# Kernel optimization log

Hardware: AMD Instinct MI355X
Metric: run time of the kernel (lower is better)

Reference implementation:

```python
import jax, jax.numpy as jnp
import numpy as np

L = 4          # num transformer layers
C = 128        # embed_dim
P = 16         # patch size
NH = 8         # num heads
HD = C // NH   # head dim
SCALE = HD ** -0.5
THRESH = [0.001, 0.0012, 0.0015, 0.002]
EPS = 1e-5


def _ln(x, w, b):
    mu = jnp.mean(x, -1, keepdims=True)
    v = jnp.mean(jnp.square(x - mu), -1, keepdims=True)
    return (x - mu) * jax.lax.rsqrt(v + EPS) * w + b


def _attn(x, qw, qb, ow, ob):
    B, N, _ = x.shape
    qkv = (x @ qw + qb).reshape(B, N, 3, NH, HD)
    q, k, v = jnp.moveaxis(qkv, 2, 0)                      # each [B,N,NH,HD]
    q = q.transpose(0, 2, 1, 3)
    k = k.transpose(0, 2, 1, 3)
    v = v.transpose(0, 2, 1, 3)                            # [B,NH,N,HD]
    probs = jax.nn.softmax(jnp.einsum('bhnd,bhmd->bhnm', q, k) * SCALE, axis=-1)
    o = jnp.einsum('bhnm,bhmd->bhnd', probs, v).transpose(0, 2, 1, 3).reshape(B, N, C)
    return o @ ow + ob, probs


def _layer(x, i, ln1_w, ln1_b, qkv_w, qkv_b, out_w, out_b, ln2_w, ln2_b, w1, b1, w2, b2):
    a, probs = _attn(_ln(x, ln1_w[i], ln1_b[i]), qkv_w[i], qkv_b[i], out_w[i], out_b[i])
    x = x + a
    h = jax.nn.gelu(_ln(x, ln2_w[i], ln2_b[i]) @ w1[i] + b1[i], approximate=False)
    return x + h @ w2[i] + b2[i], probs


def forward(conv_w, conv_b, cls_token, pos_embed, ln1_w, ln1_b, qkv_w, qkv_b,
            out_w, out_b, ln2_w, ln2_b, mlp_w1, mlp_b1, mlp_w2, mlp_b2, x, meta=None):
    B = x.shape[0]
    Hh, Ww = x.shape[2] // P, x.shape[3] // P
    # patch embed == conv with kernel=stride=P, expressed as a patch matmul
    xr = x.reshape(B, 3, Hh, P, Ww, P).transpose(0, 2, 4, 1, 3, 5).reshape(B, Hh * Ww, 3 * P * P)
    tok = xr @ conv_w.reshape(C, -1).T + conv_b           # [B, nH*nW, C]
    x = jnp.concatenate([jnp.broadcast_to(cls_token, (B, 1, C)), tok], axis=1) + pos_embed
    meta_out = []
    for i in range(L):
        x, probs = _layer(x, i, ln1_w, ln1_b, qkv_w, qkv_b, out_w, out_b,
                          ln2_w, ln2_b, mlp_w1, mlp_b1, mlp_w2, mlp_b2)
        if i < L - 1:
            cls_t, tokens = x[:, :1], x[:, 1:]
            if meta is None:
                am = jnp.mean(probs[:, :, 1:, 0], axis=1)  # [B, N] attn of tokens to cls
                keep = am > THRESH[i]
                fb = keep.sum(1) == 0                      # fallback: keep argmax token
                keep = keep | (fb[:, None] & (jnp.arange(am.shape[1])[None, :] == jnp.argmax(am, 1)[:, None]))
                count = keep.sum(1)
                order = jnp.argsort(~keep, axis=1)         # stable: kept tokens first, in order
                mk = int(jnp.max(count))
                order, count = np.asarray(order), np.asarray(count)
                meta_out.append((order, count, mk))
            else:
                order, count, mk = meta[i]
            g = jnp.take_along_axis(tokens, jnp.asarray(order[:, :mk])[:, :, None], axis=1)
            valid = (jnp.arange(mk)[None, :] < jnp.asarray(count)[:, None]).astype(tokens.dtype)
            x = jnp.concatenate([cls_t, g * valid[:, :, None]], axis=1)
            # original re-adds pos_embed[0:1+mk] regardless of which tokens survived
            x = x + jnp.concatenate([pos_embed[:, :1], pos_embed[:, 1:1 + mk]], axis=1)
    return x, meta_out


def setup_inputs() -> dict:
    key = jax.random.key(0)
    ks = jax.random.split(key, 8)
    def w(k, shape, fan_in):
        return jax.random.normal(k, shape, jnp.float32) / np.float32(np.sqrt(fan_in))
    N_POS = (512 // P) * (512 // P) + 1  # 1025
    return {
        'conv_w': w(ks[0], (C, 3, P, P), 3 * P * P),
        'conv_b': jnp.zeros((C,), jnp.float32),
        'cls_token': jnp.zeros((1, 1, C), jnp.float32),
        'pos_embed': 0.02 * jax.random.truncated_normal(ks[1], -2.0, 2.0, (1, N_POS, C), jnp.float32),
        'ln1_w': jnp.ones((L, C), jnp.float32), 'ln1_b': jnp.zeros((L, C), jnp.float32),
        'qkv_w': w(ks[2], (L, C, 3 * C), C), 'qkv_b': jnp.zeros((L, 3 * C), jnp.float32),
        'out_w': w(ks[3], (L, C, C), C), 'out_b': jnp.zeros((L, C), jnp.float32),
        'ln2_w': jnp.ones((L, C), jnp.float32), 'ln2_b': jnp.zeros((L, C), jnp.float32),
        'mlp_w1': w(ks[4], (L, C, 4 * C), C), 'mlp_b1': jnp.zeros((L, 4 * C), jnp.float32),
        'mlp_w2': w(ks[5], (L, 4 * C, C), 4 * C), 'mlp_b2': jnp.zeros((L, C), jnp.float32),
        'x': jax.random.normal(ks[6], (8, 3, 512, 512), jnp.float32),
    }


def reference(conv_w, conv_b, cls_token, pos_embed, ln1_w, ln1_b, qkv_w, qkv_b,
              out_w, out_b, ln2_w, ln2_b, mlp_w1, mlp_b1, mlp_w2, mlp_b2, x):
    out, _ = forward(conv_w, conv_b, cls_token, pos_embed, ln1_w, ln1_b, qkv_w, qkv_b,
                     out_w, out_b, ln2_w, ln2_b, mlp_w1, mlp_b1, mlp_w2, mlp_b2, x)
    return out
```

## Files before the change

kernel.cpp:

```cpp
#include <hip/hip_runtime.h>
#include <hip/hip_bf16.h>
#include <math.h>

typedef __hip_bfloat16 bf16;
typedef __attribute__((ext_vector_type(4))) _Float16 half4;
typedef __attribute__((ext_vector_type(4))) float f32x4;

#define NMAX 1025
#define TMAX 1024
#define BATCH 8
#define CH 128
#define NHEAD 8
#define HDIM 16
#define MMAX (BATCH * NMAX)
#define QTILES 65
#define VSTRIDE 1028
#define POSZ 1049600
#define KCHUNK 192

__device__ __forceinline__ float b2f(bf16 v) { return __bfloat162float(v); }

__device__ __forceinline__ bool is_bf16(const void* ln1w_raw) {
    return ((const unsigned*)ln1w_raw)[0] == 0x3F803F80u;
}
__device__ __forceinline__ float ldsel(const void* p, size_t i, bool bf) {
    return bf ? __bfloat162float(((const bf16*)p)[i]) : ((const float*)p)[i];
}

struct CvtDesc { const void* src; float* dst; int cnt; };
struct CvtPack { CvtDesc d[15]; };

__global__ void convert_kernel(CvtPack p, const void* ln1w_raw, int* nTok) {
    bool bf = is_bf16(ln1w_raw);
    CvtDesc dd = p.d[blockIdx.y];
    int idx = blockIdx.x * 256 + threadIdx.x;
    if (idx < dd.cnt) dd.dst[idx] = ldsel(dd.src, idx, bf);
    if (blockIdx.y == 0 && idx == 0) nTok[0] = NMAX;
}

__global__ void prep_kernel(const void* conv_w, float* __restrict__ wT,
                            const void* ln1w_raw) {
    bool bf = is_bf16(ln1w_raw);
    int idx = blockIdx.x * 256 + threadIdx.x;
    if (idx < 768 * 128) {
        int k = idx >> 7, oc = idx & 127;
        wT[idx] = ldsel(conv_w, (size_t)oc * 768 + k, bf);
    }
}

__global__ __launch_bounds__(256) void patch_partial(
        const void* __restrict__ img, const float* __restrict__ wT,
        float* __restrict__ partial, const void* ln1w_raw) {
    __shared__ float pbuf[8 * KCHUNK];
    bool bf = is_bf16(ln1w_raw);
    int b = blockIdx.y;
    int g = blockIdx.x & 127;
    int kc = blockIdx.x >> 7;
    int tid = threadIdx.x;
    int t0 = g * 8;
    int kbase = kc * KCHUNK;
    const int NV = 8 * KCHUNK / 4;
    for (int i = tid; i < NV; i += 256) {
        int e = i << 2;
        int t = e / KCHUNK, kloc = e - t * KCHUNK;
        int k = kbase + kloc;
        int c = k >> 8, rem = k & 255, p1 = rem >> 4, p2 = rem & 15;
        int hw = t0 + t;
        int h = hw >> 5, w = hw & 31;
        size_t a = (((size_t)(b * 3 + c) * 512) + h * 16 + p1) * 512 + w * 16 + p2;
        float4 v;
        if (bf) {
            ushort4 u = *(const ushort4*)((const unsigned short*)img + a);
            v.x = __uint_as_float((unsigned)u.x << 16);
            v.y = __uint_as_float((unsigned)u.y << 16);
            v.z = __uint_as_float((unsigned)u.z << 16);
            v.w = __uint_as_float((unsigned)u.w << 16);
        } else {
            v = *(const float4*)((const float*)img + a);
        }
        *(float4*)&pbuf[e] = v;
    }
    __syncthreads();
    int team = tid >> 7;
    int col = tid & 127;
    float acc[4];
#pragma unroll
    for (int t = 0; t < 4; t++) acc[t] = 0.f;
    const float* wc = wT + (size_t)kbase * 128;
    const float* pb = pbuf + team * 4 * KCHUNK;
    for (int k4 = 0; k4 < KCHUNK; k4 += 4) {
        float w0 = wc[(k4 + 0) * 128 + col];
        float w1 = wc[(k4 + 1) * 128 + col];
        float w2 = wc[(k4 + 2) * 128 + col];
        float w3 = wc[(k4 + 3) * 128 + col];
#pragma unroll
        for (int t = 0; t < 4; t++) {
            const float4 a = *(const float4*)&pb[t * KCHUNK + k4];
            acc[t] = fmaf(a.x, w0, acc[t]);
            acc[t] = fmaf(a.y, w1, acc[t]);
            acc[t] = fmaf(a.z, w2, acc[t]);
            acc[t] = fmaf(a.w, w3, acc[t]);
        }
    }
    float* pp = partial + ((size_t)(kc * 8 + b) * 1024 + t0 + team * 4) * 128 + col;
#pragma unroll
    for (int t = 0; t < 4; t++) pp[(size_t)t * 128] = acc[t];
}

__global__ __launch_bounds__(256) void patch_reduce(
        const float* __restrict__ partial, const float* __restrict__ conv_b,
        const float* __restrict__ cls_tok, const float* __restrict__ pos,
        float* __restrict__ out) {
    if (blockIdx.x == 4096) {
        for (int i = threadIdx.x; i < 8 * 128; i += 256) {
            int b = i >> 7, c = i & 127;
            out[(size_t)(b * NMAX) * CH + c] = cls_tok[c] + pos[c];
        }
        return;
    }
    int idx = blockIdx.x * 256 + threadIdx.x;
    int tg = idx >> 7;
    int col = idx & 127;
    int b = tg >> 10, tok = tg & 1023;
    size_t pi = ((size_t)b * 1024 + tok) * 128 + col;
    const size_t PSTRIDE = (size_t)8 * 1024 * 128;
    float v = partial[pi] + partial[pi + PSTRIDE]
            + partial[pi + 2 * PSTRIDE] + partial[pi + 3 * PSTRIDE];
    out[((size_t)(b * NMAX) + 1 + tok) * CH + col] =
        v + conv_b[col] + pos[(size_t)(1 + tok) * CH + col];
}

template <int K, int NCOL, int CTILE, int ROWS, int TEAMS, bool LN,
          bool GELU_ACT, bool RESID, bool QKV_SPLIT>
__global__ void mm_kernel(const float* __restrict__ A, const float* __restrict__ W,
                          const float* __restrict__ bias, const float* __restrict__ lnw,
                          const float* __restrict__ lnb, const float* __restrict__ R,
                          float* __restrict__ out, _Float16* __restrict__ kout,
                          _Float16* __restrict__ vout, const int* __restrict__ nPtr) {
    __shared__ float As[ROWS * K];
    const int THREADS = CTILE * TEAMS;
    const int RPT = ROWS / TEAMS;
    int N = nPtr[0];
    int M = BATCH * N;
    int row0 = blockIdx.x * ROWS;
    if (row0 >= M) return;
    int tid = threadIdx.x;
    for (int i = tid; i < ROWS * K / 4; i += THREADS) {
        int e = i << 2;
        int r = e / K, rem = e % K;
        float4 v;
        int row = row0 + r;
        if (row < M)
            v = *(const float4*)&A[(size_t)row * K + rem];
        else
            v = make_float4(0.f, 0.f, 0.f, 0.f);
        *(float4*)&As[r * K + rem] = v;
    }
    __syncthreads();
    if (LN) {
        int wid = tid >> 6, lane = tid & 63;
        const int NW = THREADS / 64;
        float wl0 = lnw[lane], wl1 = lnw[64 + lane];
        float bl0 = lnb[lane], bl1 = lnb[64 + lane];
        for (int r = wid; r < ROWS; r += NW) {
            float x0 = As[r * K + lane], x1 = As[r * K + 64 + lane];
            float s = x0 + x1;
#pragma unroll
            for (int off = 32; off; off >>= 1) s += __shfl_xor(s, off);
            float mu = s * (1.f / 128.f);
            float d0 = x0 - mu, d1 = x1 - mu;
            float v = d0 * d0 + d1 * d1;
#pragma unroll
            for (int off = 32; off; off >>= 1) v += __shfl_xor(v, off);
            float inv = 1.f / sqrtf(v * (1.f / 128.f) + 1e-5f);
            As[r * K + lane] = d0 * inv * wl0 + bl0;
            As[r * K + 64 + lane] = d1 * inv * wl1 + bl1;
        }
        __syncthreads();
    }
    int team = tid / CTILE;
    int col = tid % CTILE;
    const float* At = As + team * RPT * K;
    float acc[RPT];
#pragma unroll
    for (int r = 0; r < RPT; r++) acc[r] = 0.f;
    for (int k4 = 0; k4 < K; k4 += 4) {
        float w0 = W[(size_t)(k4 + 0) * NCOL + col];
        float w1 = W[(size_t)(k4 + 1) * NCOL + col];
        float w2 = W[(size_t)(k4 + 2) * NCOL + col];
        float w3 = W[(size_t)(k4 + 3) * NCOL + col];
#pragma unroll
        for (int r = 0; r < RPT; r++) {
            const float4 a = *(const float4*)&At[r * K + k4];
            acc[r] = fmaf(a.x, w0, acc[r]);
            acc[r] = fmaf(a.y, w1, acc[r]);
            acc[r] = fmaf(a.z, w2, acc[r]);
            acc[r] = fmaf(a.w, w3, acc[r]);
        }
    }
    float bv = bias[col];
    int rbase = row0 + team * RPT;
    int rmax = min(RPT, M - rbase);
    if (QKV_SPLIT) {
        int part = col >> 7;
        int c128 = col & 127;
        int hh = c128 >> 4, dd = c128 & 15;
        for (int r = 0; r < rmax; r++) {
            float v = acc[r] + bv;
            int row = rbase + r;
            if (part == 0) {
                out[(size_t)row * 128 + c128] = v;
            } else {
                int bb = row / N, nn = row - (row / N) * N;
                if (part == 1) {
                    _Float16 hi = (_Float16)v;
                    _Float16 lo = (_Float16)(v - (float)hi);
                    size_t kb2 = ((size_t)(bb * 8 + hh) * NMAX + nn) * 32 + dd;
                    kout[kb2] = hi;
                    kout[kb2 + 16] = lo;
                } else {
                    vout[((size_t)(bb * 8 + hh) * 16 + dd) * VSTRIDE + nn] = (_Float16)v;
                }
            }
        }
        if (blockIdx.x == 0 && part == 2) {
            int zn = min(16, VSTRIDE - N);
            for (int bb = 0; bb < 8; bb++) {
                size_t rb = ((size_t)((bb * 8 + hh) * 16 + dd)) * VSTRIDE;
                for (int i = 0; i < zn; i++) vout[rb + N + i] = (_Float16)0.f;
            }
            if (hh == 7 && dd == 15) {
                for (int i = 0; i < 16; i++)
                    vout[(size_t)1024 * VSTRIDE + i] = (_Float16)0.f;
            }
        }
    } else {
        for (int r = 0; r < rmax; r++) {
            float v = acc[r] + bv;
            if (GELU_ACT) v = 0.5f * v * (1.f + erff(v * 0.70710678118654752f));
            if (RESID) v += R[(size_t)(rbase + r) * NCOL + col];
            out[(size_t)(rbase + r) * NCOL + col] = v;
        }
    }
}

__global__ __launch_bounds__(256) void attn_kernel(
        const float* __restrict__ qbuf, const _Float16* __restrict__ kbuf,
        const _Float16* __restrict__ vbuf, float* __restrict__ oout,
        float* __restrict__ clsp, const int* __restrict__ nPtr) {
    __shared__ float sO[3][64][4];
    __shared__ float sL[3][64];
    __shared__ float sM[3][16];
    int N = nPtr[0];
    int bid = blockIdx.x;
    int b = bid & 7;
    int h = (bid >> 3) & 7;
    int qt = bid >> 6;
    if (qt * 16 >= N) return;
    int wave = threadIdx.x >> 6;
    int lane = threadIdx.x & 63;
    int ql = lane & 15;
    int hig = lane >> 4;
    int nq = qt * 16 + ql;
    int nqc = min(nq, N - 1);
    half4 qhi, qlo;
    {
        const float4 qv = *(const float4*)(qbuf + ((size_t)(b * N + nqc)) * 128 + h * HDIM + hig * 4);
        float q0 = qv.x * 0.25f, q1 = qv.y * 0.25f, q2 = qv.z * 0.25f, q3 = qv.w * 0.25f;
        qhi[0] = (_Float16)q0; qlo[0] = (_Float16)(q0 - (float)qhi[0]);
        qhi[1] = (_Float16)q1; qlo[1] = (_Float16)(q1 - (float)qhi[1]);
        qhi[2] = (_Float16)q2; qlo[2] = (_Float16)(q2 - (float)qhi[2]);
        qhi[3] = (_Float16)q3; qlo[3] = (_Float16)(q3 - (float)qhi[3]);
    }
    const _Float16* kb = kbuf + (size_t)(b * 8 + h) * NMAX * 32;
    const _Float16* vt = vbuf + ((size_t)(b * 8 + h) * 16 + ql) * VSTRIDE;
    f32x4 of = {0.f, 0.f, 0.f, 0.f};
    const f32x4 zz = {0.f, 0.f, 0.f, 0.f};
    float m = -3.0e38f, l = 0.f, s0raw = 0.f;
    int ntAll = (N + 15) >> 4;
    int ntFull = N >> 4;
    int nqt = (ntAll + 3) >> 2;
    int t0h = wave * nqt;
    int t1h = min(ntAll, t0h + nqt);
    int fullEnd = min(t1h, ntFull);
    int t = t0h;
    for (; t + 2 <= fullEnd; t += 2) {
        int k0 = t * 16;
        const _Float16* kpA = kb + ((size_t)(k0 + ql)) * 32 + hig * 4;
        const _Float16* kpB = kpA + 16 * 32;
        half4 khiA = *(const half4*)(kpA);
        half4 kloA = *(const half4*)(kpA + 16);
        half4 khiB = *(const half4*)(kpB);
        half4 kloB = *(const half4*)(kpB + 16);
        f32x4 sA1 = __builtin_amdgcn_mfma_f32_16x16x16f16(khiA, qhi, zz, 0, 0, 0);
        f32x4 sB1 = __builtin_amdgcn_mfma_f32_16x16x16f16(khiB, qhi, zz, 0, 0, 0);
        f32x4 sA2 = __builtin_amdgcn_mfma_f32_16x16x16f16(khiA, qlo, zz, 0, 0, 0);
        f32x4 sB2 = __builtin_amdgcn_mfma_f32_16x16x16f16(khiB, qlo, zz, 0, 0, 0);
        sA2 = __builtin_amdgcn_mfma_f32_16x16x16f16(kloA, qhi, sA2, 0, 0, 0);
        sB2 = __builtin_amdgcn_mfma_f32_16x16x16f16(kloB, qhi, sB2, 0, 0, 0);
        f32x4 saA = sA1 + sA2;
        f32x4 saB = sB1 + sB2;
        if (t == 0) s0raw = saA[0];
        float mcA = fmaxf(fmaxf(saA[0], saA[1]), fmaxf(saA[2], saA[3]));
        float mcB = fmaxf(fmaxf(saB[0], saB[1]), fmaxf(saB[2], saB[3]));
        float mloc = fmaxf(mcA, mcB);
        if (!__all(mloc <= m + 8.f)) {
            float mc = fmaxf(mloc, __shfl_xor(mloc, 16));
            mc = fmaxf(mc, __shfl_xor(mc, 32));
            float mnew = fmaxf(m, mc);
            float corr = __expf(m - mnew);
            l *= corr;
#pragma unroll
            for (int r = 0; r < 4; r++)
                of[r] *= __shfl(corr, hig * 4 + r);
            m = mnew;
        }
        float pA0 = __expf(saA[0] - m), pA1 = __expf(saA[1] - m);
        float pA2 = __expf(saA[2] - m), pA3 = __expf(saA[3] - m);
        float pB0 = __expf(saB[0] - m), pB1 = __expf(saB[1] - m);
        float pB2 = __expf(saB[2] - m), pB3 = __expf(saB[3] - m);
        l += ((pA0 + pA1) + (pA2 + pA3)) + ((pB0 + pB1) + (pB2 + pB3));
        half4 pfA, pfB;
        pfA[0] = (_Float16)pA0; pfA[1] = (_Float16)pA1;
        pfA[2] = (_Float16)pA2; pfA[3] = (_Float16)pA3;
        pfB[0] = (_Float16)pB0; pfB[1] = (_Float16)pB1;
        pfB[2] = (_Float16)pB2; pfB[3] = (_Float16)pB3;
        half4 vfA = *(const half4*)(vt + k0 + hig * 4);
        half4 vfB = *(const half4*)(vt + k0 + 16 + hig * 4);
        of = __builtin_amdgcn_mfma_f32_16x16x16f16(pfA, vfA, of, 0, 0, 0);
        of = __builtin_amdgcn_mfma_f32_16x16x16f16(pfB, vfB, of, 0, 0, 0);
    }
    if (t < fullEnd) {
        int k0 = t * 16;
        const _Float16* kp = kb + ((size_t)(k0 + ql)) * 32 + hig * 4;
        half4 khi = *(const half4*)(kp);
        half4 klo = *(const half4*)(kp + 16);
        f32x4 s1 = __builtin_amdgcn_mfma_f32_16x16x16f16(khi, qhi, zz, 0, 0, 0);
        f32x4 s2 = __builtin_amdgcn_mfma_f32_16x16x16f16(khi, qlo, zz, 0, 0, 0);
        s2 = __builtin_amdgcn_mfma_f32_16x16x16f16(klo, qhi, s2, 0, 0, 0);
        f32x4 sa = s1 + s2;
        if (t == 0) s0raw = sa[0];
        float mloc = fmaxf(fmaxf(sa[0], sa[1]), fmaxf(sa[2], sa[3]));
        if (!__all(mloc <= m + 8.f)) {
            float mc = fmaxf(mloc, __shfl_xor(mloc, 16));
            mc = fmaxf(mc, __shfl_xor(mc, 32));
            float mnew = fmaxf(m, mc);
            float corr = __expf(m - mnew);
            l *= corr;
#pragma unroll
            for (int r = 0; r < 4; r++)
                of[r] *= __shfl(corr, hig * 4 + r);
            m = mnew;
        }
        float p0 = __expf(sa[0] - m), p1 = __expf(sa[1] - m);
        float p2 = __expf(sa[2] - m), p3 = __expf(sa[3] - m);
        l += (p0 + p1) + (p2 + p3);
        half4 pf;
        pf[0] = (_Float16)p0; pf[1] = (_Float16)p1;
        pf[2] = (_Float16)p2; pf[3] = (_Float16)p3;
        half4 vf = *(const half4*)(vt + k0 + hig * 4);
        of = __builtin_amdgcn_mfma_f32_16x16x16f16(pf, vf, of, 0, 0, 0);
        t++;
    }
    if (t < t1h) {
        int k0t = t * 16;
        int kk = min(k0t + ql, N - 1);
        const _Float16* kp = kb + (size_t)kk * 32 + hig * 4;
        half4 khi = *(const half4*)(kp);
        half4 klo = *(const half4*)(kp + 16);
        f32x4 s1 = __builtin_amdgcn_mfma_f32_16x16x16f16(khi, qhi, zz, 0, 0, 0);
        f32x4 s2 = __builtin_amdgcn_mfma_f32_16x16x16f16(khi, qlo, zz, 0, 0, 0);
        s2 = __builtin_amdgcn_mfma_f32_16x16x16f16(klo, qhi, s2, 0, 0, 0);
        f32x4 sa = s1 + s2;
        if (t == 0) s0raw = sa[0];
        float s0 = (k0t + hig * 4 + 0 < N) ? sa[0] : -3.0e38f;
        float s1m = (k0t + hig * 4 + 1 < N) ? sa[1] : -3.0e38f;
        float s2m = (k0t + hig * 4 + 2 < N) ? sa[2] : -3.0e38f;
        float s3m = (k0t + hig * 4 + 3 < N) ? sa[3] : -3.0e38f;
        float mloc = fmaxf(fmaxf(s0, s1m), fmaxf(s2m, s3m));
        if (!__all(mloc <= m + 8.f)) {
            float mc = fmaxf(mloc, __shfl_xor(mloc, 16));
            mc = fmaxf(mc, __shfl_xor(mc, 32));
            float mnew = fmaxf(m, mc);
            float corr = __expf(m - mnew);
            l *= corr;
#pragma unroll
            for (int r = 0; r < 4; r++)
                of[r] *= __shfl(corr, hig * 4 + r);
            m = mnew;
        }
        float p0 = __expf(s0 - m);
        float p1 = __expf(s1m - m);
        float p2 = __expf(s2m - m);
        float p3 = __expf(s3m - m);
        l += (p0 + p1) + (p2 + p3);
        half4 pf;
        pf[0] = (_Float16)p0; pf[1] = (_Float16)p1;
        pf[2] = (_Float16)p2; pf[3] = (_Float16)p3;
        half4 vf = *(const half4*)(vt + k0t + hig * 4);
        of = __builtin_amdgcn_mfma_f32_16x16x16f16(pf, vf, of, 0, 0, 0);
    }
    l += __shfl_xor(l, 16);
    l += __shfl_xor(l, 32);
    if (wave != 0) {
        if (hig == 0) sM[wave - 1][ql] = m;
        sL[wave - 1][lane] = l;
        sO[wave - 1][lane][0] = of[0];
        sO[wave - 1][lane][1] = of[1];
        sO[wave - 1][lane][2] = of[2];
        sO[wave - 1][lane][3] = of[3];
    }
    __syncthreads();
    if (wave == 0) {
        float m1 = sM[0][ql], m2 = sM[1][ql], m3 = sM[2][ql];
        float M = fmaxf(fmaxf(m, m1), fmaxf(m2, m3));
        float w0 = __expf(m - M), w1 = __expf(m1 - M);
        float w2 = __expf(m2 - M), w3 = __expf(m3 - M);
        float L = w0 * l + w1 * sL[0][lane] + w2 * sL[1][lane] + w3 * sL[2][lane];
        float linv = 1.f / L;
#pragma unroll
        for (int r = 0; r < 4; r++) {
            int qs = hig * 4 + r;
            float W0 = __shfl(w0, qs);
            float W1 = __shfl(w1, qs);
            float W2 = __shfl(w2, qs);
            float W3 = __shfl(w3, qs);
            float Li = __shfl(linv, qs);
            int qq = qt * 16 + qs;
            if (qq < N) {
                float ov = W0 * of[r] + W1 * sO[0][lane][r]
                         + W2 * sO[1][lane][r] + W3 * sO[2][lane][r];
                oout[((size_t)(b * N + qq)) * 128 + h * HDIM + ql] = ov * Li;
            }
        }
        if (hig == 0 && nq >= 1 && nq < N) {
            clsp[(size_t)(b * 8 + h) * TMAX + (nq - 1)] =
                __expf(s0raw - m) * w0 * linv;
        }
    }
}

__global__ __launch_bounds__(1024) void prune_kernel(const float* __restrict__ clsp,
                                                     int* __restrict__ order,
                                                     int* __restrict__ cnt,
                                                     const int* __restrict__ nPtr, int layer) {
    __shared__ int sdata[1024];
    __shared__ float wv_[16];
    __shared__ int wi_[16];
    __shared__ int wc_[16];
    __shared__ int sArg, sCnt0;
    int b = blockIdx.x;
    int t = threadIdx.x;
    int N = nPtr[0];
    int T = N - 1;
    float am = -1.f;
    if (t < T) {
        float s = 0.f;
#pragma unroll
        for (int h = 0; h < 8; h++) s += clsp[((size_t)(b * 8 + h)) * TMAX + t];
        am = s * 0.125f;
    }
    const double TH[4] = {0.001, 0.0012, 0.0015, 0.002};
    int keep = (t < T) && ((double)am > TH[layer]);
    float bv = am;
    int bi = t;
    int kc = keep;
#pragma unroll
    for (int off = 32; off; off >>= 1) {
        float ov = __shfl_xor(bv, off);
        int oi = __shfl_xor(bi, off);
        if (ov > bv || (ov == bv && oi < bi)) { bv = ov; bi = oi; }
        kc += __shfl_xor(kc, off);
    }
    int wid = t >> 6, lane = t & 63;
    if (lane == 0) { wv_[wid] = bv; wi_[wid] = bi; wc_[wid] = kc; }
    __syncthreads();
    if (t == 0) {
        float Bv = wv_[0];
        int Bi = wi_[0], C = 0;
        for (int w = 0; w < 16; w++) {
            C += wc_[w];
            if (wv_[w] > Bv || (wv_[w] == Bv && wi_[w] < Bi)) { Bv = wv_[w]; Bi = wi_[w]; }
        }
        sArg = Bi;
        sCnt0 = C;
    }
    __syncthreads();
    if (sCnt0 == 0) keep = (t == sArg) && (t < T);
    sdata[t] = keep;
    __syncthreads();
    for (int off = 1; off < 1024; off <<= 1) {
        int v = sdata[t];
        int add = (t >= off) ? sdata[t - off] : 0;
        __syncthreads();
        sdata[t] = v + add;
        __syncthreads();
    }
    int incl = sdata[t];
    int total = sdata[1023];
    if (t < T) {
        if (keep)
            order[b * TMAX + (incl - 1)] = t;
        else
            order[b * TMAX + total + t - incl] = t;
    }
    if (t == 0) cnt[b] = total;
}

__global__ __launch_bounds__(256) void gather_kernel(
        const float* __restrict__ xin, float* __restrict__ xout,
        const int* __restrict__ order, const int* __restrict__ cnt,
        const float* __restrict__ pos, const int* __restrict__ nPtr,
        int* __restrict__ nNext) {
    int Nold = nPtr[0];
    int mk = cnt[0];
#pragma unroll
    for (int i = 1; i < 8; i++) mk = max(mk, cnt[i]);
    int Nnew = mk + 1;
    if (blockIdx.x == 0 && blockIdx.y == 0 && threadIdx.x == 0) nNext[0] = Nnew;
    int b = blockIdx.y;
    int j = blockIdx.x * 2 + (threadIdx.x >> 7);
    int c = threadIdx.x & 127;
    if (j >= Nnew) return;
    float v;
    if (j == 0)
        v = xin[((size_t)(b * Nold)) * CH + c];
    else {
        int src = order[b * TMAX + (j - 1)];
        v = (j - 1 < cnt[b]) ? xin[((size_t)(b * Nold + 1 + src)) * CH + c] : 0.f;
    }
    xout[((size_t)(b * Nnew + j)) * CH + c] = v + pos[(size_t)j * CH + c];
}

__global__ void outconv_kernel(const float* __restrict__ xin, void* __restrict__ out,
                               int total, const void* ln1w_raw) {
    bool bf = is_bf16(ln1w_raw);
    int i = blockIdx.x * 256 + threadIdx.x;
    if (i < total) {
        if (bf) ((bf16*)out)[i] = __float2bfloat16(xin[i]);
        else    ((float*)out)[i] = xin[i];
    }
}

extern "C" void kernel_launch(void* const* d_in, const int* in_sizes, int n_in,
                              void* d_out, int out_size, void* d_ws, size_t ws_size,
                              hipStream_t stream) {
    const void* conv_w = d_in[0];
    const void* conv_b = d_in[1];
    const void* cls_token = d_in[2];
    const void* pos_embed = d_in[3];
    const void* ln1_w = d_in[4];
    const void* ln1_b = d_in[5];
    const void* qkv_w = d_in[6];
    const void* qkv_b = d_in[7];
    const void* out_w = d_in[8];
    const void* out_b = d_in[9];
    const void* ln2_w = d_in[10];
    const void* ln2_b = d_in[11];
    const void* mlp_w1 = d_in[12];
    const void* mlp_b1 = d_in[13];
    const void* mlp_w2 = d_in[14];
    const void* mlp_b2 = d_in[15];
    const void* img = d_in[16];

    float* ws = (float*)d_ws;
    size_t off = 0;
    float* bufA = ws + off; off += POSZ;
    float* bufB = ws + off; off += POSZ;
    float* obuf = ws + off; off += POSZ;
    float* tmp  = ws + off; off += (size_t)BATCH * NMAX * 512;
    float* wT   = ws + off; off += 768 * 128;
    float* clsp = ws + off; off += (size_t)BATCH * NHEAD * TMAX;
    int* order  = (int*)(ws + off); off += BATCH * TMAX;
    int* cnt    = (int*)(ws + off); off += 16;
    int* nTok   = (int*)(ws + off); off += 16;
    float* wts  = ws + off;
    const size_t wts_total = 924544;

    float* qbuf = tmp;
    _Float16* kbuf = (_Float16*)(tmp + POSZ);
    _Float16* vbuf = (_Float16*)(tmp + 2 * POSZ);

    float* f_conv_b = wts + 0;
    float* f_cls    = wts + 128;
    float* f_pos    = wts + 256;
    float* f_ln1w   = wts + 131456;
    float* f_ln1b   = wts + 131968;
    float* f_qkvw   = wts + 132480;
    float* f_qkvb   = wts + 329088;
    float* f_outw   = wts + 330624;
    float* f_outb   = wts + 396160;
    float* f_ln2w   = wts + 396672;
    float* f_ln2b   = wts + 397184;
    float* f_w1     = wts + 397696;
    float* f_b1     = wts + 659840;
    float* f_w2     = wts + 661888;
    float* f_b2     = wts + 924032;

    CvtPack pk;
    pk.d[0]  = {conv_b,    f_conv_b, 128};
    pk.d[1]  = {cls_token, f_cls,    128};
    pk.d[2]  = {pos_embed, f_pos,    131200};
    pk.d[3]  = {ln1_w,     f_ln1w,   512};
    pk.d[4]  = {ln1_b,     f_ln1b,   512};
    pk.d[5]  = {qkv_w,     f_qkvw,   196608};
    pk.d[6]  = {qkv_b,     f_qkvb,   1536};
    pk.d[7]  = {out_w,     f_outw,   65536};
    pk.d[8]  = {out_b,     f_outb,   512};
    pk.d[9]  = {ln2_w,     f_ln2w,   512};
    pk.d[10] = {ln2_b,     f_ln2b,   512};
    pk.d[11] = {mlp_w1,    f_w1,     262144};
    pk.d[12] = {mlp_b1,    f_b1,     2048};
    pk.d[13] = {mlp_w2,    f_w2,     262144};
    pk.d[14] = {mlp_b2,    f_b2,     512};

    convert_kernel<<<dim3(1024, 15), 256, 0, stream>>>(pk, ln1_w, nTok);
    prep_kernel<<<(768 * 128 + 255) / 256, 256, 0, stream>>>(conv_w, wT, ln1_w);
    patch_partial<<<dim3(512, BATCH), 256, 0, stream>>>(img, wT, tmp, ln1_w);
    patch_reduce<<<4097, 256, 0, stream>>>(tmp, f_conv_b, f_cls, f_pos, bufA);

    float* xc = bufA;
    float* xalt = bufB;
    const int GR8 = (MMAX + 7) / 8;

    for (int i = 0; i < 4; i++) {
        const int* nP = nTok + i;
        mm_kernel<128, 384, 384, 8, 1, true, false, false, true>
            <<<GR8, 384, 0, stream>>>(
            xc, f_qkvw + (size_t)i * 128 * 384, f_qkvb + i * 384,
            f_ln1w + i * 128, f_ln1b + i * 128, nullptr, qbuf, kbuf, vbuf, nP);
        attn_kernel<<<QTILES * 64, 256, 0, stream>>>(
            qbuf, kbuf, vbuf, qbuf, clsp, nP);
        mm_kernel<128, 128, 128, 8, 2, false, false, true, false>
            <<<GR8, 256, 0, stream>>>(
            qbuf, f_outw + (size_t)i * 128 * 128, f_outb + i * 128,
            nullptr, nullptr, xc, xalt, nullptr, nullptr, nP);
        mm_kernel<128, 512, 512, 8, 1, true, true, false, false>
            <<<GR8, 512, 0, stream>>>(
            xalt, f_w1 + (size_t)i * 128 * 512, f_b1 + i * 512,
            f_ln2w + i * 128, f_ln2b + i * 128, nullptr, tmp, nullptr, nullptr, nP);
        mm_kernel<512, 128, 128, 8, 2, false, false, true, false>
            <<<GR8, 256, 0, stream>>>(
            tmp, f_w2 + (size_t)i * 512 * 128, f_b2 + i * 128,
            nullptr, nullptr, xalt, xc, nullptr, nullptr, nP);
        if (i < 3) {
            prune_kernel<<<BATCH, 1024, 0, stream>>>(clsp, order, cnt, nP, i);
            gather_kernel<<<dim3((NMAX + 1) / 2, BATCH), 256, 0, stream>>>(
                xc, xalt, order, cnt, f_pos, nP, nTok + i + 1);
            float* t2 = xc; xc = xalt; xalt = t2;
        }
    }
    outconv_kernel<<<(out_size + 255) / 256, 256, 0, stream>>>(xc, d_out, out_size, ln1_w);
}
```

Baseline: 562.5 us.

## Process two query tiles per attention block to reuse K/V loads

Each attention block now handles a pair of 16-query tiles, sharing every K and V fragment load between both tiles' MFMA score and PV computations. The grid is halved and the cross-wave merge state in shared memory is doubled. This cuts redundant K/V global reads and per-block overhead, at the cost of more registers per thread and fewer blocks for latency hiding.

```diff
diff --git a/kernel.cpp b/kernel.cpp
--- a/kernel.cpp
+++ b/kernel.cpp
@@ -13,7 +13,7 @@
 #define NHEAD 8
 #define HDIM 16
 #define MMAX (BATCH * NMAX)
-#define QTILES 65
+#define QPAIRS 33
 #define VSTRIDE 1028
 #define POSZ 1049600
 #define KCHUNK 192
@@ -248,35 +248,97 @@
         const float* __restrict__ qbuf, const _Float16* __restrict__ kbuf,
         const _Float16* __restrict__ vbuf, float* __restrict__ oout,
         float* __restrict__ clsp, const int* __restrict__ nPtr) {
-    __shared__ float sO[3][64][4];
-    __shared__ float sL[3][64];
-    __shared__ float sM[3][16];
+    __shared__ float sO[3][2][64][4];
+    __shared__ float sL[3][2][64];
+    __shared__ float sM[3][2][16];
     int N = nPtr[0];
     int bid = blockIdx.x;
     int b = bid & 7;
     int h = (bid >> 3) & 7;
-    int qt = bid >> 6;
-    if (qt * 16 >= N) return;
+    int qp = bid >> 6;
+    int qt0 = qp * 2, qt1 = qp * 2 + 1;
+    if (qt0 * 16 >= N) return;
     int wave = threadIdx.x >> 6;
     int lane = threadIdx.x & 63;
     int ql = lane & 15;
     int hig = lane >> 4;
-    int nq = qt * 16 + ql;
-    int nqc = min(nq, N - 1);
-    half4 qhi, qlo;
+    int nq0 = qt0 * 16 + ql;
+    int nq1 = qt1 * 16 + ql;
+    half4 qhi0, qlo0, qhi1, qlo1;
     {
+        int nqc = min(nq0, N - 1);
         const float4 qv = *(const float4*)(qbuf + ((size_t)(b * N + nqc)) * 128 + h * HDIM + hig * 4);
         float q0 = qv.x * 0.25f, q1 = qv.y * 0.25f, q2 = qv.z * 0.25f, q3 = qv.w * 0.25f;
-        qhi[0] = (_Float16)q0; qlo[0] = (_Float16)(q0 - (float)qhi[0]);
-        qhi[1] = (_Float16)q1; qlo[1] = (_Float16)(q1 - (float)qhi[1]);
-        qhi[2] = (_Float16)q2; qlo[2] = (_Float16)(q2 - (float)qhi[2]);
-        qhi[3] = (_Float16)q3; qlo[3] = (_Float16)(q3 - (float)qhi[3]);
+        qhi0[0] = (_Float16)q0; qlo0[0] = (_Float16)(q0 - (float)qhi0[0]);
+        qhi0[1] = (_Float16)q1; qlo0[1] = (_Float16)(q1 - (float)qhi0[1]);
+        qhi0[2] = (_Float16)q2; qlo0[2] = (_Float16)(q2 - (float)qhi0[2]);
+        qhi0[3] = (_Float16)q3; qlo0[3] = (_Float16)(q3 - (float)qhi0[3]);
+    }
+    {
+        int nqc = min(nq1, N - 1);
+        const float4 qv = *(const float4*)(qbuf + ((size_t)(b * N + nqc)) * 128 + h * HDIM + hig * 4);
+        float q0 = qv.x * 0.25f, q1 = qv.y * 0.25f, q2 = qv.z * 0.25f, q3 = qv.w * 0.25f;
+        qhi1[0] = (_Float16)q0; qlo1[0] = (_Float16)(q0 - (float)qhi1[0]);
+        qhi1[1] = (_Float16)q1; qlo1[1] = (_Float16)(q1 - (float)qhi1[1]);
+        qhi1[2] = (_Float16)q2; qlo1[2] = (_Float16)(q2 - (float)qhi1[2]);
+        qhi1[3] = (_Float16)q3; qlo1[3] = (_Float16)(q3 - (float)qhi1[3]);
     }
     const _Float16* kb = kbuf + (size_t)(b * 8 + h) * NMAX * 32;
     const _Float16* vt = vbuf + ((size_t)(b * 8 + h) * 16 + ql) * VSTRIDE;
-    f32x4 of = {0.f, 0.f, 0.f, 0.f};
+    f32x4 of0 = {0.f, 0.f, 0.f, 0.f};
+    f32x4 of1 = {0.f, 0.f, 0.f, 0.f};
     const f32x4 zz = {0.f, 0.f, 0.f, 0.f};
-    float m = -3.0e38f, l = 0.f, s0raw = 0.f;
+    float m0 = -3.0e38f, l0 = 0.f, m1 = -3.0e38f, l1 = 0.f;
+    float s0raw0 = 0.f, s0raw1 = 0.f;
+    auto upd2 = [&](float& m, float& l, f32x4& of, f32x4 sa, f32x4 sb,
+                    half4 vfA, half4 vfB) {
+        float mloc = fmaxf(fmaxf(fmaxf(sa[0], sa[1]), fmaxf(sa[2], sa[3])),
+                           fmaxf(fmaxf(sb[0], sb[1]), fmaxf(sb[2], sb[3])));
+        if (!__all(mloc <= m + 8.f)) {
+            float mc = fmaxf(mloc, __shfl_xor(mloc, 16));
+            mc = fmaxf(mc, __shfl_xor(mc, 32));
+            float mnew = fmaxf(m, mc);
+            float corr = __expf(m - mnew);
+            l *= corr;
+#pragma unroll
+            for (int r = 0; r < 4; r++)
+                of[r] *= __shfl(corr, hig * 4 + r);
+            m = mnew;
+        }
+        float pA0 = __expf(sa[0] - m), pA1 = __expf(sa[1] - m);
+        float pA2 = __expf(sa[2] - m), pA3 = __expf(sa[3] - m);
+        float pB0 = __expf(sb[0] - m), pB1 = __expf(sb[1] - m);
+        float pB2 = __expf(sb[2] - m), pB3 = __expf(sb[3] - m);
+        l += ((pA0 + pA1) + (pA2 + pA3)) + ((pB0 + pB1) + (pB2 + pB3));
+        half4 pfA, pfB;
+        pfA[0] = (_Float16)pA0; pfA[1] = (_Float16)pA1;
+        pfA[2] = (_Float16)pA2; pfA[3] = (_Float16)pA3;
+        pfB[0] = (_Float16)pB0; pfB[1] = (_Float16)pB1;
+        pfB[2] = (_Float16)pB2; pfB[3] = (_Float16)pB3;
+        of = __builtin_amdgcn_mfma_f32_16x16x16f16(pfA, vfA, of, 0, 0, 0);
+        of = __builtin_amdgcn_mfma_f32_16x16x16f16(pfB, vfB, of, 0, 0, 0);
+    };
+    auto upd1 = [&](float& m, float& l, f32x4& of, f32x4 sa, half4 vf) {
+        float mloc = fmaxf(fmaxf(sa[0], sa[1]), fmaxf(sa[2], sa[3]));
+        if (!__all(mloc <= m + 8.f)) {
+            float mc = fmaxf(mloc, __shfl_xor(mloc, 16));
+            mc = fmaxf(mc, __shfl_xor(mc, 32));
+            float mnew = fmaxf(m, mc);
+            float corr = __expf(m - mnew);
+            l *= corr;
+#pragma unroll
+            for (int r = 0; r < 4; r++)
+                of[r] *= __shfl(corr, hig * 4 + r);
+            m = mnew;
+        }
+        float p0 = __expf(sa[0] - m), p1 = __expf(sa[1] - m);
+        float p2 = __expf(sa[2] - m), p3 = __expf(sa[3] - m);
+        l += (p0 + p1) + (p2 + p3);
+        half4 pf;
+        pf[0] = (_Float16)p0; pf[1] = (_Float16)p1;
+        pf[2] = (_Float16)p2; pf[3] = (_Float16)p3;
+        of = __builtin_amdgcn_mfma_f32_16x16x16f16(pf, vf, of, 0, 0, 0);
+    };
     int ntAll = (N + 15) >> 4;
     int ntFull = N >> 4;
     int nqt = (ntAll + 3) >> 2;
@@ -292,74 +354,39 @@
         half4 kloA = *(const half4*)(kpA + 16);
         half4 khiB = *(const half4*)(kpB);
         half4 kloB = *(const half4*)(kpB + 16);
-        f32x4 sA1 = __builtin_amdgcn_mfma_f32_16x16x16f16(khiA, qhi, zz, 0, 0, 0);
-        f32x4 sB1 = __builtin_amdgcn_mfma_f32_16x16x16f16(khiB, qhi, zz, 0, 0, 0);
-        f32x4 sA2 = __builtin_amdgcn_mfma_f32_16x16x16f16(khiA, qlo, zz, 0, 0, 0);
-        f32x4 sB2 = __builtin_amdgcn_mfma_f32_16x16x16f16(khiB, qlo, zz, 0, 0, 0);
-        sA2 = __builtin_amdgcn_mfma_f32_16x16x16f16(kloA, qhi, sA2, 0, 0, 0);
-        sB2 = __builtin_amdgcn_mfma_f32_16x16x16f16(kloB, qhi, sB2, 0, 0, 0);
-        f32x4 saA = sA1 + sA2;
-        f32x4 saB = sB1 + sB2;
-        if (t == 0) s0raw = saA[0];
-        float mcA = fmaxf(fmaxf(saA[0], saA[1]), fmaxf(saA[2], saA[3]));
-        float mcB = fmaxf(fmaxf(saB[0], saB[1]), fmaxf(saB[2], saB[3]));
-        float mloc = fmaxf(mcA, mcB);
-        if (!__all(mloc <= m + 8.f)) {
-            float mc = fmaxf(mloc, __shfl_xor(mloc, 16));
-            mc = fmaxf(mc, __shfl_xor(mc, 32));
-            float mnew = fmaxf(m, mc);
-            float corr = __expf(m - mnew);
-            l *= corr;
-#pragma unroll
-            for (int r = 0; r < 4; r++)
-                of[r] *= __shfl(corr, hig * 4 + r);
-            m = mnew;
-        }
-        float pA0 = __expf(saA[0] - m), pA1 = __expf(saA[1] - m);
-        float pA2 = __expf(saA[2] - m), pA3 = __expf(saA[3] - m);
-        float pB0 = __expf(saB[0] - m), pB1 = __expf(saB[1] - m);
-        float pB2 = __expf(saB[2] - m), pB3 = __expf(saB[3] - m);
-        l += ((pA0 + pA1) + (pA2 + pA3)) + ((pB0 + pB1) + (pB2 + pB3));
-        half4 pfA, pfB;
-        pfA[0] = (_Float16)pA0; pfA[1] = (_Float16)pA1;
-        pfA[2] = (_Float16)pA2; pfA[3] = (_Float16)pA3;
-        pfB[0] = (_Float16)pB0; pfB[1] = (_Float16)pB1;
-        pfB[2] = (_Float16)pB2; pfB[3] = (_Float16)pB3;
+        f32x4 saA0 = __builtin_amdgcn_mfma_f32_16x16x16f16(khiA, qhi0, zz, 0, 0, 0);
+        f32x4 saB0 = __builtin_amdgcn_mfma_f32_16x16x16f16(khiB, qhi0, zz, 0, 0, 0);
+        f32x4 saA1 = __builtin_amdgcn_mfma_f32_16x16x16f16(khiA, qhi1, zz, 0, 0, 0);
+        f32x4 saB1 = __builtin_amdgcn_mfma_f32_16x16x16f16(khiB, qhi1, zz, 0, 0, 0);
+        saA0 = __builtin_amdgcn_mfma_f32_16x16x16f16(khiA, qlo0, saA0, 0, 0, 0);
+        saB0 = __builtin_amdgcn_mfma_f32_16x16x16f16(khiB, qlo0, saB0, 0, 0, 0);
+        saA1 = __builtin_amdgcn_mfma_f32_16x16x16f16(khiA, qlo1, saA1, 0, 0, 0);
+        saB1 = __builtin_amdgcn_mfma_f32_16x16x16f16(khiB, qlo1, saB1, 0, 0, 0);
+        saA0 = __builtin_amdgcn_mfma_f32_16x16x16f16(kloA, qhi0, saA0, 0, 0, 0);
+        saB0 = __builtin_amdgcn_mfma_f32_16x16x16f16(kloB, qhi0, saB0, 0, 0, 0);
+        saA1 = __builtin_amdgcn_mfma_f32_16x16x16f16(kloA, qhi1, saA1, 0, 0, 0);
+        saB1 = __builtin_amdgcn_mfma_f32_16x16x16f16(kloB, qhi1, saB1, 0, 0, 0);
+        if (t == 0) { s0raw0 = saA0[0]; s0raw1 = saA1[0]; }
         half4 vfA = *(const half4*)(vt + k0 + hig * 4);
         half4 vfB = *(const half4*)(vt + k0 + 16 + hig * 4);
-        of = __builtin_amdgcn_mfma_f32_16x16x16f16(pfA, vfA, of, 0, 0, 0);
-        of = __builtin_amdgcn_mfma_f32_16x16x16f16(pfB, vfB, of, 0, 0, 0);
+        upd2(m0, l0, of0, saA0, saB0, vfA, vfB);
+        upd2(m1, l1, of1, saA1, saB1, vfA, vfB);
     }
     if (t < fullEnd) {
         int k0 = t * 16;
         const _Float16* kp = kb + ((size_t)(k0 + ql)) * 32 + hig * 4;
         half4 khi = *(const half4*)(kp);
         half4 klo = *(const half4*)(kp + 16);
-        f32x4 s1 = __builtin_amdgcn_mfma_f32_16x16x16f16(khi, qhi, zz, 0, 0, 0);
-        f32x4 s2 = __builtin_amdgcn_mfma_f32_16x16x16f16(khi, qlo, zz, 0, 0, 0);
-        s2 = __builtin_amdgcn_mfma_f32_16x16x16f16(klo, qhi, s2, 0, 0, 0);
-        f32x4 sa = s1 + s2;
-        if (t == 0) s0raw = sa[0];
-        float mloc = fmaxf(fmaxf(sa[0], sa[1]), fmaxf(sa[2], sa[3]));
-        if (!__all(mloc <= m + 8.f)) {
-            float mc = fmaxf(mloc, __shfl_xor(mloc, 16));
-            mc = fmaxf(mc, __shfl_xor(mc, 32));
-            float mnew = fmaxf(m, mc);
-            float corr = __expf(m - mnew);
-            l *= corr;
-#pragma unroll
-            for (int r = 0; r < 4; r++)
-                of[r] *= __shfl(corr, hig * 4 + r);
-            m = mnew;
-        }
-        float p0 = __expf(sa[0] - m), p1 = __expf(sa[1] - m);
-        float p2 = __expf(sa[2] - m), p3 = __expf(sa[3] - m);
-        l += (p0 + p1) + (p2 + p3);
-        half4 pf;
-        pf[0] = (_Float16)p0; pf[1] = (_Float16)p1;
-        pf[2] = (_Float16)p2; pf[3] = (_Float16)p3;
+        f32x4 sa0 = __builtin_amdgcn_mfma_f32_16x16x16f16(khi, qhi0, zz, 0, 0, 0);
+        f32x4 sa1 = __builtin_amdgcn_mfma_f32_16x16x16f16(khi, qhi1, zz, 0, 0, 0);
+        sa0 = __builtin_amdgcn_mfma_f32_16x16x16f16(khi, qlo0, sa0, 0, 0, 0);
+        sa1 = __builtin_amdgcn_mfma_f32_16x16x16f16(khi, qlo1, sa1, 0, 0, 0);
+        sa0 = __builtin_amdgcn_mfma_f32_16x16x16f16(klo, qhi0, sa0, 0, 0, 0);
+        sa1 = __builtin_amdgcn_mfma_f32_16x16x16f16(klo, qhi1, sa1, 0, 0, 0);
+        if (t == 0) { s0raw0 = sa0[0]; s0raw1 = sa1[0]; }
         half4 vf = *(const half4*)(vt + k0 + hig * 4);
-        of = __builtin_amdgcn_mfma_f32_16x16x16f16(pf, vf, of, 0, 0, 0);
+        upd1(m0, l0, of0, sa0, vf);
+        upd1(m1, l1, of1, sa1, vf);
         t++;
     }
     if (t < t1h) {
@@ -368,75 +395,73 @@
         const _Float16* kp = kb + (size_t)kk * 32 + hig * 4;
         half4 khi = *(const half4*)(kp);
         half4 klo = *(const half4*)(kp + 16);
-        f32x4 s1 = __builtin_amdgcn_mfma_f32_16x16x16f16(khi, qhi, zz, 0, 0, 0);
-        f32x4 s2 = __builtin_amdgcn_mfma_f32_16x16x16f16(khi, qlo, zz, 0, 0, 0);
-        s2 = __builtin_amdgcn_mfma_f32_16x16x16f16(klo, qhi, s2, 0, 0, 0);
-        f32x4 sa = s1 + s2;
-        if (t == 0) s0raw = sa[0];
-        float s0 = (k0t + hig * 4 + 0 < N) ? sa[0] : -3.0e38f;
-        float s1m = (k0t + hig * 4 + 1 < N) ? sa[1] : -3.0e38f;
-        float s2m = (k0t + hig * 4 + 2 < N) ? sa[2] : -3.0e38f;
-        float s3m = (k0t + hig * 4 + 3 < N) ? sa[3] : -3.0e38f;
-        float mloc = fmaxf(fmaxf(s0, s1m), fmaxf(s2m, s3m));
-        if (!__all(mloc <= m + 8.f)) {
-            float mc = fmaxf(mloc, __shfl_xor(mloc, 16));
-            mc = fmaxf(mc, __shfl_xor(mc, 32));
-            float mnew = fmaxf(m, mc);
-            float corr = __expf(m - mnew);
-            l *= corr;
-#pragma unroll
-            for (int r = 0; r < 4; r++)
-                of[r] *= __shfl(corr, hig * 4 + r);
-            m = mnew;
-        }
-        float p0 = __expf(s0 - m);
-        float p1 = __expf(s1m - m);
-        float p2 = __expf(s2m - m);
-        float p3 = __expf(s3m - m);
-        l += (p0 + p1) + (p2 + p3);
-        half4 pf;
-        pf[0] = (_Float16)p0; pf[1] = (_Float16)p1;
-        pf[2] = (_Float16)p2; pf[3] = (_Float16)p3;
+        f32x4 sa0 = __builtin_amdgcn_mfma_f32_16x16x16f16(khi, qhi0, zz, 0, 0, 0);
+        f32x4 sa1 = __builtin_amdgcn_mfma_f32_16x16x16f16(khi, qhi1, zz, 0, 0, 0);
+        sa0 = __builtin_amdgcn_mfma_f32_16x16x16f16(khi, qlo0, sa0, 0, 0, 0);
+        sa1 = __builtin_amdgcn_mfma_f32_16x16x16f16(khi, qlo1, sa1, 0, 0, 0);
+        sa0 = __builtin_amdgcn_mfma_f32_16x16x16f16(klo, qhi0, sa0, 0, 0, 0);
+        sa1 = __builtin_amdgcn_mfma_f32_16x16x16f16(klo, qhi1, sa1, 0, 0, 0);
+        if (t == 0) { s0raw0 = sa0[0]; s0raw1 = sa1[0]; }
+#pragma unroll
+        for (int r = 0; r < 4; r++) {
+            bool in = (k0t + hig * 4 + r) < N;
+            sa0[r] = in ? sa0[r] : -3.0e38f;
+            sa1[r] = in ? sa1[r] : -3.0e38f;
+        }
         half4 vf = *(const half4*)(vt + k0t + hig * 4);
-        of = __builtin_amdgcn_mfma_f32_16x16x16f16(pf, vf, of, 0, 0, 0);
-    }
-    l += __shfl_xor(l, 16);
-    l += __shfl_xor(l, 32);
+        upd1(m0, l0, of0, sa0, vf);
+        upd1(m1, l1, of1, sa1, vf);
+    }
+    l0 += __shfl_xor(l0, 16);
+    l0 += __shfl_xor(l0, 32);
+    l1 += __shfl_xor(l1, 16);
+    l1 += __shfl_xor(l1, 32);
     if (wave != 0) {
-        if (hig == 0) sM[wave - 1][ql] = m;
-        sL[wave - 1][lane] = l;
-        sO[wave - 1][lane][0] = of[0];
-        sO[wave - 1][lane][1] = of[1];
-        sO[wave - 1][lane][2] = of[2];
-        sO[wave - 1][lane][3] = of[3];
+        if (hig == 0) {
+            sM[wave - 1][0][ql] = m0;
+            sM[wave - 1][1][ql] = m1;
+        }
+        sL[wave - 1][0][lane] = l0;
+        sL[wave - 1][1][lane] = l1;
+#pragma unroll
+        for (int r = 0; r < 4; r++) {
+            sO[wave - 1][0][lane][r] = of0[r];
+            sO[wave - 1][1][lane][r] = of1[r];
+        }
     }
     __syncthreads();
     if (wave == 0) {
-        float m1 = sM[0][ql], m2 = sM[1][ql], m3 = sM[2][ql];
-        float M = fmaxf(fmaxf(m, m1), fmaxf(m2, m3));
-        float w0 = __expf(m - M), w1 = __expf(m1 - M);
-        float w2 = __expf(m2 - M), w3 = __expf(m3 - M);
-        float L = w0 * l + w1 * sL[0][lane] + w2 * sL[1][lane] + w3 * sL[2][lane];
-        float linv = 1.f / L;
-#pragma unroll
-        for (int r = 0; r < 4; r++) {
-            int qs = hig * 4 + r;
-            float W0 = __shfl(w0, qs);
-            float W1 = __shfl(w1, qs);
-            float W2 = __shfl(w2, qs);
-            float W3 = __shfl(w3, qs);
-            float Li = __shfl(linv, qs);
-            int qq = qt * 16 + qs;
-            if (qq < N) {
-                float ov = W0 * of[r] + W1 * sO[0][lane][r]
-                         + W2 * sO[1][lane][r] + W3 * sO[2][lane][r];
-                oout[((size_t)(b * N + qq)) * 128 + h * HDIM + ql] = ov * Li;
+        auto mergeOne = [&](int j, float m, float l, f32x4 of, float s0raw, int qt) {
+            float ma = sM[0][j][ql], mb = sM[1][j][ql], mc = sM[2][j][ql];
+            float M = fmaxf(fmaxf(m, ma), fmaxf(mb, mc));
+            float w0 = __expf(m - M), w1 = __expf(ma - M);
+            float w2 = __expf(mb - M), w3 = __expf(mc - M);
+            float L = w0 * l + w1 * sL[0][j][lane] + w2 * sL[1][j][lane]
+                    + w3 * sL[2][j][lane];
+            float linv = 1.f / L;
+#pragma unroll
+            for (int r = 0; r < 4; r++) {
+                int qs = hig * 4 + r;
+                float W0 = __shfl(w0, qs);
+                float W1 = __shfl(w1, qs);
+                float W2 = __shfl(w2, qs);
+                float W3 = __shfl(w3, qs);
+                float Li = __shfl(linv, qs);
+                int qq = qt * 16 + qs;
+                if (qq < N) {
+                    float ov = W0 * of[r] + W1 * sO[0][j][lane][r]
+                             + W2 * sO[1][j][lane][r] + W3 * sO[2][j][lane][r];
+                    oout[((size_t)(b * N + qq)) * 128 + h * HDIM + ql] = ov * Li;
+                }
             }
-        }
-        if (hig == 0 && nq >= 1 && nq < N) {
-            clsp[(size_t)(b * 8 + h) * TMAX + (nq - 1)] =
-                __expf(s0raw - m) * w0 * linv;
-        }
+            int nq = qt * 16 + ql;
+            if (hig == 0 && nq >= 1 && nq < N) {
+                clsp[(size_t)(b * 8 + h) * TMAX + (nq - 1)] =
+                    __expf(s0raw - m) * w0 * linv;
+            }
+        };
+        mergeOne(0, m0, l0, of0, s0raw0, qt0);
+        mergeOne(1, m1, l1, of1, s0raw1, qt1);
     }
 }
 
@@ -629,7 +654,7 @@
             <<<GR8, 384, 0, stream>>>(
             xc, f_qkvw + (size_t)i * 128 * 384, f_qkvb + i * 384,
             f_ln1w + i * 128, f_ln1b + i * 128, nullptr, qbuf, kbuf, vbuf, nP);
-        attn_kernel<<<QTILES * 64, 256, 0, stream>>>(
+        attn_kernel<<<QPAIRS * 64, 256, 0, stream>>>(
             qbuf, kbuf, vbuf, qbuf, clsp, nP);
         mm_kernel<128, 128, 128, 8, 2, false, false, true, false>
             <<<GR8, 256, 0, stream>>>(
```

Result: faster. 546.0 us, median of 2 (-2.9%).
